# Optimization experiments

Hardware: AMD Instinct MI355X
Metric: run time of the kernel (lower is better)

## Reference

```python
import jax, jax.numpy as jnp
import numpy as np

B, T, E, A = 4, 4096, 256, 64

def setup_inputs() -> dict:
    key = jax.random.key(0)
    ks = jax.random.split(key, 7)
    s = 1.0 / np.sqrt(E)
    return {
        "embedded": jax.random.normal(ks[0], (B, T, E), dtype=jnp.float32),
        "Wk": jax.random.normal(ks[1], (E, A), dtype=jnp.float32) * s,
        "bk": jax.random.normal(ks[2], (A,), dtype=jnp.float32) * s,
        "Wq": jax.random.normal(ks[3], (E, A), dtype=jnp.float32) * s,
        "bq": jax.random.normal(ks[4], (A,), dtype=jnp.float32) * s,
        "Wv": jax.random.normal(ks[5], (E, A), dtype=jnp.float32) * s,
        "bv": jax.random.normal(ks[6], (A,), dtype=jnp.float32) * s,
    }

def reference(embedded, Wk, bk, Wq, bq, Wv, bv):
    k = embedded @ Wk + bk                      # [B,T,A]
    q = embedded @ Wq + bq
    v = embedded @ Wv + bv
    scale = 1.0 / jnp.sqrt(jnp.asarray(k.shape[-1], dtype=k.dtype))
    scores = jnp.einsum('bqa,bka->bqk', q, k) * scale   # [B,T,T]
    Tn = scores.shape[-1]
    causal = jnp.tril(jnp.ones((Tn, Tn), dtype=bool))
    scores = jnp.where(causal, scores, -jnp.inf)
    sm = jax.nn.softmax(scores, axis=-1)
    return jnp.einsum('bqk,bka->bqa', sm, v)            # [B,T,A]
```

## Files before the change

kernel.cpp:

```cpp
#include <hip/hip_runtime.h>
#include <math.h>

#define Bn 4
#define Tn 4096
#define En 256
#define An 64
#define PLS 72
#define WLS 264

typedef __attribute__((ext_vector_type(8))) short short8;
typedef __attribute__((ext_vector_type(8))) __bf16 bf16x8;
typedef __attribute__((ext_vector_type(4))) float f32x4;
typedef __attribute__((ext_vector_type(4))) short short4v;
typedef __attribute__((ext_vector_type(2))) unsigned int uint2v;

__device__ __forceinline__ f32x4 mfma16(short8 a, short8 b, f32x4 c) {
    return __builtin_amdgcn_mfma_f32_16x16x32_bf16(
        __builtin_bit_cast(bf16x8, a), __builtin_bit_cast(bf16x8, b), c, 0, 0, 0);
}
__device__ __forceinline__ unsigned short f2bf(float x) {
    unsigned int u = __builtin_bit_cast(unsigned int, x);
    u += 0x7fffu + ((u >> 16) & 1u);
    return (unsigned short)(u >> 16);
}
__device__ __forceinline__ float bf2f(unsigned short h) {
    return __builtin_bit_cast(float, (unsigned int)h << 16);
}
__device__ __forceinline__ unsigned int packbf2(float lo, float hi) {
    return (unsigned int)f2bf(lo) | ((unsigned int)f2bf(hi) << 16);
}

__global__ __launch_bounds__(256, 2) void proj_kernel(
    const float* __restrict__ emb,
    const float* __restrict__ Wq, const float* __restrict__ Wk, const float* __restrict__ Wv,
    const float* __restrict__ bq, const float* __restrict__ bk, const float* __restrict__ bv,
    unsigned short* __restrict__ qg, unsigned short* __restrict__ kg,
    unsigned short* __restrict__ v_t)
{
    const int bid  = blockIdx.x;
    const int tid  = threadIdx.x;
    const int wave = tid >> 6, lane = tid & 63, quad = lane >> 4, l15 = lane & 15;
    const int jh   = bid & 1;
    const int rb   = bid >> 1;
    const int row0  = rb * 64;
    const int b     = row0 >> 12;
    const int trow0 = row0 & 4095;

    __shared__ unsigned short Wl[96 * WLS];
    __shared__ unsigned short vtr[64 * PLS];

    {
        const float* __restrict__ srcA = jh ? Wv : Wq;
        const int lrbA = jh ? 32 : 0;
#pragma unroll
        for (int it = 0; it < 16; it++) {
            const int idx = it * 256 + tid;
            const int e   = idx >> 4;
            const int c4  = (idx & 15) * 4;
            float4 w = *(const float4*)&srcA[(size_t)e * An + c4];
            Wl[(lrbA + c4 + 0) * WLS + e] = f2bf(w.x);
            Wl[(lrbA + c4 + 1) * WLS + e] = f2bf(w.y);
            Wl[(lrbA + c4 + 2) * WLS + e] = f2bf(w.z);
            Wl[(lrbA + c4 + 3) * WLS + e] = f2bf(w.w);
        }
        const int coloff = jh ? 32 : 0;
        const int lrbB   = jh ? 0 : 64;
#pragma unroll
        for (int it = 0; it < 8; it++) {
            const int idx = it * 256 + tid;
            const int e   = idx >> 3;
            const int c4  = (idx & 7) * 4;
            float4 w = *(const float4*)&Wk[(size_t)e * An + coloff + c4];
            Wl[(lrbB + c4 + 0) * WLS + e] = f2bf(w.x);
            Wl[(lrbB + c4 + 1) * WLS + e] = f2bf(w.y);
            Wl[(lrbB + c4 + 2) * WLS + e] = f2bf(w.z);
            Wl[(lrbB + c4 + 3) * WLS + e] = f2bf(w.w);
        }
    }

    short8 A[8];
    {
        const float* erow = emb + (size_t)(row0 + wave * 16 + l15) * En;
#pragma unroll
        for (int c = 0; c < 8; c++) {
            const float* pp = erow + c * 32 + quad * 8;
            float4 f0 = *(const float4*)pp;
            float4 f1 = *(const float4*)(pp + 4);
            A[c] = (short8){(short)f2bf(f0.x), (short)f2bf(f0.y), (short)f2bf(f0.z), (short)f2bf(f0.w),
                            (short)f2bf(f1.x), (short)f2bf(f1.y), (short)f2bf(f1.z), (short)f2bf(f1.w)};
        }
    }
    __syncthreads();

    f32x4 acc[6];
#pragma unroll
    for (int x = 0; x < 6; x++) acc[x] = (f32x4){0.f, 0.f, 0.f, 0.f};

#pragma unroll
    for (int x = 0; x < 6; x++) {
        const unsigned short* wrow = &Wl[(x * 16 + l15) * WLS];
#pragma unroll
        for (int c = 0; c < 8; c++)
            acc[x] = mfma16(A[c], *(const short8*)(wrow + c * 32 + quad * 8), acc[x]);
    }

    const float QS = 0.125f * 1.4426950408889634f;
    const int row_l = wave * 16 + quad * 4;

    if (jh == 0) {
        __syncthreads();
#pragma unroll
        for (int x = 0; x < 4; x++) {
            const int al = x * 16 + l15;
            const float bsv = bq[al];
#pragma unroll
            for (int rg = 0; rg < 4; rg++)
                vtr[(row_l + rg) * PLS + al] = f2bf((acc[x][rg] + bsv) * QS);
        }
        __syncthreads();
        if (tid < 128) {
            const int row = tid >> 1, cg = (tid & 1) * 32;
            unsigned short* dst = qg + (size_t)(row0 + row) * An + cg;
            *(short8*)dst       = *(const short8*)&vtr[row * PLS + cg];
            *(short8*)(dst + 8) = *(const short8*)&vtr[row * PLS + cg + 8];
            *(short8*)(dst + 16) = *(const short8*)&vtr[row * PLS + cg + 16];
            *(short8*)(dst + 24) = *(const short8*)&vtr[row * PLS + cg + 24];
        }
        __syncthreads();
#pragma unroll
        for (int x = 4; x < 6; x++) {
            const int al = (x - 4) * 16 + l15;
            const float bsv = bk[al];
#pragma unroll
            for (int rg = 0; rg < 4; rg++)
                vtr[(row_l + rg) * PLS + al] = f2bf(acc[x][rg] + bsv);
        }
        __syncthreads();
        if (tid < 64) {
            const int row = tid;
            unsigned short* dst = kg + (size_t)(row0 + row) * An;
            *(short8*)dst       = *(const short8*)&vtr[row * PLS];
            *(short8*)(dst + 8) = *(const short8*)&vtr[row * PLS + 8];
            *(short8*)(dst + 16) = *(const short8*)&vtr[row * PLS + 16];
            *(short8*)(dst + 24) = *(const short8*)&vtr[row * PLS + 24];
        }
    } else {
        __syncthreads();
#pragma unroll
        for (int x = 0; x < 2; x++) {
            const int al = (2 + x) * 16 + l15;
            const float bsv = bk[al];
#pragma unroll
            for (int rg = 0; rg < 4; rg++)
                vtr[(row_l + rg) * PLS + al] = f2bf(acc[x][rg] + bsv);
        }
        __syncthreads();
        if (tid < 64) {
            const int row = tid;
            unsigned short* dst = kg + (size_t)(row0 + row) * An + 32;
            *(short8*)dst       = *(const short8*)&vtr[row * PLS + 32];
            *(short8*)(dst + 8) = *(const short8*)&vtr[row * PLS + 40];
            *(short8*)(dst + 16) = *(const short8*)&vtr[row * PLS + 48];
            *(short8*)(dst + 24) = *(const short8*)&vtr[row * PLS + 56];
        }
        __syncthreads();
#pragma unroll
        for (int x = 2; x < 6; x++) {
            const int al = (x - 2) * 16 + l15;
            const float bsv = bv[al];
#pragma unroll
            for (int rg = 0; rg < 4; rg++)
                vtr[al * PLS + row_l + rg] = f2bf(acc[x][rg] + bsv);
        }
        __syncthreads();
        {
            const int a  = tid >> 2;
            const int tg = (tid & 3) * 16;
            unsigned short* dst = v_t + (size_t)(b * 64 + a) * Tn + trow0 + tg;
            *(short8*)dst       = *(const short8*)&vtr[a * PLS + tg];
            *(short8*)(dst + 8) = *(const short8*)&vtr[a * PLS + tg + 8];
        }
    }
}

__global__ __launch_bounds__(256, 2) void flash_kernel(
    const unsigned short* __restrict__ qg, const unsigned short* __restrict__ kg,
    const unsigned short* __restrict__ v_t,
    unsigned short* __restrict__ Opart, float* __restrict__ ml,
    int S, int lgS)
{
    const int b    = blockIdx.y;
    const int tid  = threadIdx.x;
    const int wave = tid >> 6, lane = tid & 63, quad = lane >> 4, l15 = lane & 15;
    const int u    = blockIdx.x * 4 + wave;
    const int p    = u >> lgS;
    const int s    = u & (S - 1);

    __shared__ unsigned short lds[4 * 64 * PLS];
    unsigned short* tw = lds + wave * (64 * PLS);

    const unsigned short* kb0 = kg  + ((size_t)b << 12) * An;
    const unsigned short* vb0 = v_t + (size_t)b * An * Tn;

#pragma unroll 1
    for (int tile = 0; tile < 2; tile++) {
        const int qt    = tile ? (63 - p) : p;
        const int qrow0 = qt * 64;
        const int tmax  = qt;

        short8 qB[4][2];
        {
            const unsigned short* qb = qg + (((size_t)b << 12) + qrow0) * An;
#pragma unroll
            for (int g = 0; g < 4; g++)
#pragma unroll
                for (int c = 0; c < 2; c++)
                    qB[g][c] = *(const short8*)(qb + (size_t)(16 * g + l15) * An + c * 32 + quad * 8);
        }

        float l_lane[4] = {0.f, 0.f, 0.f, 0.f};
        f32x4 O[4][4];
#pragma unroll
        for (int nt = 0; nt < 4; nt++)
#pragma unroll
            for (int g = 0; g < 4; g++) O[nt][g] = (f32x4){0.f, 0.f, 0.f, 0.f};

        int t = s;
        if (t <= tmax) {
            short8 KA[4][2];
            {
                const unsigned short* kb = kb0 + (size_t)t * (64 * An);
#pragma unroll
                for (int nt = 0; nt < 4; nt++)
#pragma unroll
                    for (int c = 0; c < 2; c++)
                        KA[nt][c] = *(const short8*)(kb + (nt * 16 + l15) * An + c * 32 + quad * 8);
            }
            for (;;) {
                short8 VA[4][2];
                {
                    const unsigned short* vb = vb0 + (size_t)t * 64;
#pragma unroll
                    for (int nt = 0; nt < 4; nt++)
#pragma unroll
                        for (int c = 0; c < 2; c++)
                            VA[nt][c] = *(const short8*)(vb + (size_t)(nt * 16 + l15) * Tn + c * 32 + quad * 8);
                }

                const int tn = t + S;
                const bool more = (tn <= tmax);
                short8 KN[4][2];
                if (more) {
                    const unsigned short* kb = kb0 + (size_t)tn * (64 * An);
#pragma unroll
                    for (int nt = 0; nt < 4; nt++)
#pragma unroll
                        for (int c = 0; c < 2; c++)
                            KN[nt][c] = *(const short8*)(kb + (nt * 16 + l15) * An + c * 32 + quad * 8);
                }

                const bool diag = (t == tmax);

#pragma unroll
                for (int g = 0; g < 4; g++) {
                    f32x4 St[4];
#pragma unroll
                    for (int nt = 0; nt < 4; nt++) {
                        f32x4 a0 = (f32x4){0.f, 0.f, 0.f, 0.f};
                        a0 = mfma16(KA[nt][0], qB[g][0], a0);
                        a0 = mfma16(KA[nt][1], qB[g][1], a0);
                        St[nt] = a0;
                    }
                    if (diag) {
                        const int qr = 16 * g + l15;
                        const int kvb = quad * 4;
#pragma unroll
                        for (int nt = 0; nt < 4; nt++)
#pragma unroll
                            for (int rg = 0; rg < 4; rg++)
                                if (nt * 16 + kvb + rg > qr) St[nt][rg] = -__builtin_inff();
                    }
                    float rs = l_lane[g];
#pragma unroll
                    for (int nt = 0; nt < 4; nt++) {
#pragma unroll
                        for (int rg = 0; rg < 4; rg++) {
                            const float pv = exp2f(St[nt][rg]);
                            St[nt][rg] = pv;
                            rs += pv;
                        }
                        const unsigned int d0 = packbf2(St[nt][0], St[nt][1]);
                        const unsigned int d1 = packbf2(St[nt][2], St[nt][3]);
                        *(short4v*)&tw[(16 * g + l15) * PLS + 16 * nt + quad * 4] =
                            __builtin_bit_cast(short4v, (uint2v){d0, d1});
                    }
                    l_lane[g] = rs;
#pragma unroll
                    for (int c = 0; c < 2; c++) {
                        const short8 pb = *(const short8*)&tw[(16 * g + l15) * PLS + c * 32 + quad * 8];
#pragma unroll
                        for (int nt = 0; nt < 4; nt++)
                            O[nt][g] = mfma16(VA[nt][c], pb, O[nt][g]);
                    }
                }

                if (!more) break;
                t = tn;
#pragma unroll
                for (int nt = 0; nt < 4; nt++)
#pragma unroll
                    for (int c = 0; c < 2; c++) KA[nt][c] = KN[nt][c];
            }
        }

        float l_red[4];
#pragma unroll
        for (int g = 0; g < 4; g++) {
            float rs = l_lane[g];
            rs += __shfl_xor(rs, 16);
            rs += __shfl_xor(rs, 32);
            l_red[g] = rs;
        }
#pragma unroll
        for (int nt = 0; nt < 4; nt++)
#pragma unroll
            for (int g = 0; g < 4; g++) {
                const unsigned int d0 = packbf2(O[nt][g][0], O[nt][g][1]);
                const unsigned int d1 = packbf2(O[nt][g][2], O[nt][g][3]);
                *(short4v*)&tw[(16 * g + l15) * PLS + 16 * nt + quad * 4] =
                    __builtin_bit_cast(short4v, (uint2v){d0, d1});
            }
        {
            const size_t unit = (size_t)(b * 64 + qt) * (size_t)S + s;
            unsigned short* ob = Opart + unit * 4096;
#pragma unroll
            for (int rr = 0; rr < 2; rr++) {
                const int row = rr * 32 + (lane >> 1);
#pragma unroll
                for (int pp = 0; pp < 4; pp++) {
                    const int colh = (lane & 1) * 8 + pp * 16;
                    *(short8*)(ob + row * 64 + colh) = *(const short8*)&tw[row * PLS + colh];
                }
            }
            if (quad == 0) {
                float* mlb = ml + unit * 64;
#pragma unroll
                for (int g = 0; g < 4; g++)
                    mlb[16 * g + l15] = l_red[g];
            }
        }
    }
}

__global__ __launch_bounds__(256) void merge_kernel(
    const unsigned short* __restrict__ Opart, const float* __restrict__ ml,
    float* __restrict__ out, int S)
{
    const int qt = blockIdx.x, b = blockIdx.y;
    const int tid = threadIdx.x;
    const int qr  = tid >> 2;
    const int a16 = (tid & 3) * 16;
    const size_t ub = (size_t)(b * 64 + qt) * (size_t)S;

    float acc[16];
#pragma unroll
    for (int x = 0; x < 16; x++) acc[x] = 0.f;
    float lsum = 0.f;

#pragma unroll 1
    for (int s = 0; s < S; s++) {
        lsum += ml[(ub + s) * 64 + qr];
        const unsigned short* op = &Opart[(ub + s) * 4096 + qr * 64 + a16];
        const short8 o0 = *(const short8*)op;
        const short8 o1 = *(const short8*)(op + 8);
#pragma unroll
        for (int x = 0; x < 8; x++) {
            acc[x]     += bf2f((unsigned short)o0[x]);
            acc[8 + x] += bf2f((unsigned short)o1[x]);
        }
    }
    const float inv = 1.f / lsum;
    float* o = out + (((size_t)b << 12) + qt * 64 + qr) * An + a16;
#pragma unroll
    for (int h = 0; h < 4; h++) {
        float4 r = {acc[h * 4] * inv, acc[h * 4 + 1] * inv,
                    acc[h * 4 + 2] * inv, acc[h * 4 + 3] * inv};
        *(float4*)(o + h * 4) = r;
    }
}

extern "C" void kernel_launch(void* const* d_in, const int* in_sizes, int n_in,
                              void* d_out, int out_size, void* d_ws, size_t ws_size,
                              hipStream_t stream) {
    const float* emb = (const float*)d_in[0];
    const float* Wk  = (const float*)d_in[1];
    const float* bk  = (const float*)d_in[2];
    const float* Wq  = (const float*)d_in[3];
    const float* bq  = (const float*)d_in[4];
    const float* Wv  = (const float*)d_in[5];
    const float* bv  = (const float*)d_in[6];
    float* out = (float*)d_out;

    char* ws = (char*)d_ws;
    const size_t MB = 1024 * 1024;

    int S = 8, lgS = 3;
    {
        const size_t need16 = 6 * MB + 64 * 1024
                            + (size_t)16 * 64 * 1024
                            + (size_t)16 * 2 * MB;
        if (need16 <= ws_size) { S = 16; lgS = 4; }
    }

    unsigned short* q     = (unsigned short*)(ws);
    unsigned short* k     = (unsigned short*)(ws + 2 * MB);
    unsigned short* v_t   = (unsigned short*)(ws + 4 * MB);
    float*          ml    = (float*)(ws + 6 * MB + 64 * 1024);
    unsigned short* Opart = (unsigned short*)(ws + 6 * MB + 64 * 1024 + (size_t)S * 64 * 1024);

    proj_kernel<<<512, 256, 0, stream>>>(emb, Wq, Wk, Wv, bq, bk, bv, q, k, v_t);
    flash_kernel<<<dim3(8 * S, 4), 256, 0, stream>>>(q, k, v_t, Opart, ml, S, lgS);
    merge_kernel<<<dim3(64, 4), 256, 0, stream>>>(Opart, ml, out, S);
}
```

Before: 144.6 us.

## Shrink flash query tiles to 32 rows, keep P in registers with fp16 PV MFMA

The flash kernel now works on 32-row query tiles instead of 64, which doubles the number of work units and raises occupancy to 4 blocks per SM via launch bounds. V is stored as fp16 so the PV product can use the 16x16x16 f16 MFMA with P taken straight from the score accumulator registers, removing the LDS round-trip used to transpose P. Block indices are remapped to interleave batches, and the explicit K prefetch of the next tile is dropped. The merge kernel and workspace sizing are adapted to the 32-row partials. Risks include fp16 range for V and P, the loss of K prefetch overlap, and the lower-throughput K=16 MFMA.

```diff
diff --git a/kernel.cpp b/kernel.cpp
--- a/kernel.cpp
+++ b/kernel.cpp
@@ -12,11 +12,15 @@
 typedef __attribute__((ext_vector_type(8))) __bf16 bf16x8;
 typedef __attribute__((ext_vector_type(4))) float f32x4;
 typedef __attribute__((ext_vector_type(4))) short short4v;
+typedef __attribute__((ext_vector_type(4))) _Float16 f16x4;
 typedef __attribute__((ext_vector_type(2))) unsigned int uint2v;
 
 __device__ __forceinline__ f32x4 mfma16(short8 a, short8 b, f32x4 c) {
     return __builtin_amdgcn_mfma_f32_16x16x32_bf16(
         __builtin_bit_cast(bf16x8, a), __builtin_bit_cast(bf16x8, b), c, 0, 0, 0);
+}
+__device__ __forceinline__ f32x4 mfma16h(f16x4 a, f16x4 b, f32x4 c) {
+    return __builtin_amdgcn_mfma_f32_16x16x16f16(a, b, c, 0, 0, 0);
 }
 __device__ __forceinline__ unsigned short f2bf(float x) {
     unsigned int u = __builtin_bit_cast(unsigned int, x);
@@ -28,6 +32,10 @@
 }
 __device__ __forceinline__ unsigned int packbf2(float lo, float hi) {
     return (unsigned int)f2bf(lo) | ((unsigned int)f2bf(hi) << 16);
+}
+__device__ __forceinline__ unsigned short f2h(float x) {
+    _Float16 h = (_Float16)x;
+    return __builtin_bit_cast(unsigned short, h);
 }
 
 __global__ __launch_bounds__(256, 2) void proj_kernel(
@@ -121,8 +129,8 @@
         if (tid < 128) {
             const int row = tid >> 1, cg = (tid & 1) * 32;
             unsigned short* dst = qg + (size_t)(row0 + row) * An + cg;
-            *(short8*)dst       = *(const short8*)&vtr[row * PLS + cg];
-            *(short8*)(dst + 8) = *(const short8*)&vtr[row * PLS + cg + 8];
+            *(short8*)dst        = *(const short8*)&vtr[row * PLS + cg];
+            *(short8*)(dst + 8)  = *(const short8*)&vtr[row * PLS + cg + 8];
             *(short8*)(dst + 16) = *(const short8*)&vtr[row * PLS + cg + 16];
             *(short8*)(dst + 24) = *(const short8*)&vtr[row * PLS + cg + 24];
         }
@@ -139,8 +147,8 @@
         if (tid < 64) {
             const int row = tid;
             unsigned short* dst = kg + (size_t)(row0 + row) * An;
-            *(short8*)dst       = *(const short8*)&vtr[row * PLS];
-            *(short8*)(dst + 8) = *(const short8*)&vtr[row * PLS + 8];
+            *(short8*)dst        = *(const short8*)&vtr[row * PLS];
+            *(short8*)(dst + 8)  = *(const short8*)&vtr[row * PLS + 8];
             *(short8*)(dst + 16) = *(const short8*)&vtr[row * PLS + 16];
             *(short8*)(dst + 24) = *(const short8*)&vtr[row * PLS + 24];
         }
@@ -158,8 +166,8 @@
         if (tid < 64) {
             const int row = tid;
             unsigned short* dst = kg + (size_t)(row0 + row) * An + 32;
-            *(short8*)dst       = *(const short8*)&vtr[row * PLS + 32];
-            *(short8*)(dst + 8) = *(const short8*)&vtr[row * PLS + 40];
+            *(short8*)dst        = *(const short8*)&vtr[row * PLS + 32];
+            *(short8*)(dst + 8)  = *(const short8*)&vtr[row * PLS + 40];
             *(short8*)(dst + 16) = *(const short8*)&vtr[row * PLS + 48];
             *(short8*)(dst + 24) = *(const short8*)&vtr[row * PLS + 56];
         }
@@ -170,7 +178,7 @@
             const float bsv = bv[al];
 #pragma unroll
             for (int rg = 0; rg < 4; rg++)
-                vtr[al * PLS + row_l + rg] = f2bf(acc[x][rg] + bsv);
+                vtr[al * PLS + row_l + rg] = f2h(acc[x][rg] + bsv);
         }
         __syncthreads();
         {
@@ -183,50 +191,52 @@
     }
 }
 
-__global__ __launch_bounds__(256, 2) void flash_kernel(
+__global__ __launch_bounds__(256, 4) void flash_kernel(
     const unsigned short* __restrict__ qg, const unsigned short* __restrict__ kg,
     const unsigned short* __restrict__ v_t,
     unsigned short* __restrict__ Opart, float* __restrict__ ml,
     int S, int lgS)
 {
-    const int b    = blockIdx.y;
+    const int bid  = blockIdx.x;
     const int tid  = threadIdx.x;
     const int wave = tid >> 6, lane = tid & 63, quad = lane >> 4, l15 = lane & 15;
-    const int u    = blockIdx.x * 4 + wave;
+    const int b    = (bid & 7) >> 1;
+    const int idx  = (bid >> 3) * 2 + (bid & 1);
+    const int u    = idx * 4 + wave;
     const int p    = u >> lgS;
     const int s    = u & (S - 1);
 
-    __shared__ unsigned short lds[4 * 64 * PLS];
-    unsigned short* tw = lds + wave * (64 * PLS);
+    __shared__ unsigned short lds[4 * 32 * PLS];
+    unsigned short* tw = lds + wave * (32 * PLS);
 
     const unsigned short* kb0 = kg  + ((size_t)b << 12) * An;
     const unsigned short* vb0 = v_t + (size_t)b * An * Tn;
 
 #pragma unroll 1
     for (int tile = 0; tile < 2; tile++) {
-        const int qt    = tile ? (63 - p) : p;
-        const int qrow0 = qt * 64;
-        const int tmax  = qt;
-
-        short8 qB[4][2];
+        const int qt32  = tile ? (127 - p) : p;
+        const int qrow0 = qt32 * 32;
+        const int tmax  = qt32 >> 1;
+
+        short8 qB[2][2];
         {
             const unsigned short* qb = qg + (((size_t)b << 12) + qrow0) * An;
 #pragma unroll
-            for (int g = 0; g < 4; g++)
+            for (int g = 0; g < 2; g++)
 #pragma unroll
                 for (int c = 0; c < 2; c++)
                     qB[g][c] = *(const short8*)(qb + (size_t)(16 * g + l15) * An + c * 32 + quad * 8);
         }
 
-        float l_lane[4] = {0.f, 0.f, 0.f, 0.f};
-        f32x4 O[4][4];
+        float l_lane[2] = {0.f, 0.f};
+        f32x4 O[4][2];
 #pragma unroll
         for (int nt = 0; nt < 4; nt++)
 #pragma unroll
-            for (int g = 0; g < 4; g++) O[nt][g] = (f32x4){0.f, 0.f, 0.f, 0.f};
-
-        int t = s;
-        if (t <= tmax) {
+            for (int g = 0; g < 2; g++) O[nt][g] = (f32x4){0.f, 0.f, 0.f, 0.f};
+
+#pragma unroll 1
+        for (int t = s; t <= tmax; t += S) {
             short8 KA[4][2];
             {
                 const unsigned short* kb = kb0 + (size_t)t * (64 * An);
@@ -236,86 +246,70 @@
                     for (int c = 0; c < 2; c++)
                         KA[nt][c] = *(const short8*)(kb + (nt * 16 + l15) * An + c * 32 + quad * 8);
             }
-            for (;;) {
-                short8 VA[4][2];
-                {
-                    const unsigned short* vb = vb0 + (size_t)t * 64;
+
+            f32x4 St[4][2];
+#pragma unroll
+            for (int nt = 0; nt < 4; nt++)
+#pragma unroll
+                for (int g = 0; g < 2; g++) {
+                    f32x4 a0 = (f32x4){0.f, 0.f, 0.f, 0.f};
+                    a0 = mfma16(KA[nt][0], qB[g][0], a0);
+                    a0 = mfma16(KA[nt][1], qB[g][1], a0);
+                    St[nt][g] = a0;
+                }
+
+            f16x4 VA[4][4];
+            {
+                const unsigned short* vb = vb0 + (size_t)t * 64 + quad * 4;
+#pragma unroll
+                for (int nt = 0; nt < 4; nt++)
+#pragma unroll
+                    for (int kc = 0; kc < 4; kc++)
+                        VA[nt][kc] = *(const f16x4*)(vb + (size_t)(nt * 16 + l15) * Tn + kc * 16);
+            }
+
+            if (t == tmax) {
+                const int kvb = t * 64 + quad * 4;
+#pragma unroll
+                for (int nt = 0; nt < 4; nt++)
+#pragma unroll
+                    for (int g = 0; g < 2; g++) {
+                        const int qr = qrow0 + 16 * g + l15;
+#pragma unroll
+                        for (int rg = 0; rg < 4; rg++)
+                            if (kvb + nt * 16 + rg > qr) St[nt][g][rg] = -__builtin_inff();
+                    }
+            }
+
+#pragma unroll
+            for (int g = 0; g < 2; g++) {
+                float rs = l_lane[g];
+#pragma unroll
+                for (int nt = 0; nt < 4; nt++)
+#pragma unroll
+                    for (int rg = 0; rg < 4; rg++) {
+                        const float pv = exp2f(St[nt][g][rg]);
+                        St[nt][g][rg] = pv;
+                        rs += pv;
+                    }
+                l_lane[g] = rs;
+            }
+
+#pragma unroll
+            for (int kc = 0; kc < 4; kc++)
+#pragma unroll
+                for (int g = 0; g < 2; g++) {
+                    const f16x4 pb = { (_Float16)St[kc][g][0], (_Float16)St[kc][g][1],
+                                       (_Float16)St[kc][g][2], (_Float16)St[kc][g][3] };
 #pragma unroll
                     for (int nt = 0; nt < 4; nt++)
-#pragma unroll
-                        for (int c = 0; c < 2; c++)
-                            VA[nt][c] = *(const short8*)(vb + (size_t)(nt * 16 + l15) * Tn + c * 32 + quad * 8);
+                        O[nt][g] = mfma16h(VA[nt][kc], pb, O[nt][g]);
                 }
-
-                const int tn = t + S;
-                const bool more = (tn <= tmax);
-                short8 KN[4][2];
-                if (more) {
-                    const unsigned short* kb = kb0 + (size_t)tn * (64 * An);
-#pragma unroll
-                    for (int nt = 0; nt < 4; nt++)
-#pragma unroll
-                        for (int c = 0; c < 2; c++)
-                            KN[nt][c] = *(const short8*)(kb + (nt * 16 + l15) * An + c * 32 + quad * 8);
-                }
-
-                const bool diag = (t == tmax);
-
-#pragma unroll
-                for (int g = 0; g < 4; g++) {
-                    f32x4 St[4];
-#pragma unroll
-                    for (int nt = 0; nt < 4; nt++) {
-                        f32x4 a0 = (f32x4){0.f, 0.f, 0.f, 0.f};
-                        a0 = mfma16(KA[nt][0], qB[g][0], a0);
-                        a0 = mfma16(KA[nt][1], qB[g][1], a0);
-                        St[nt] = a0;
-                    }
-                    if (diag) {
-                        const int qr = 16 * g + l15;
-                        const int kvb = quad * 4;
-#pragma unroll
-                        for (int nt = 0; nt < 4; nt++)
-#pragma unroll
-                            for (int rg = 0; rg < 4; rg++)
-                                if (nt * 16 + kvb + rg > qr) St[nt][rg] = -__builtin_inff();
-                    }
-                    float rs = l_lane[g];
-#pragma unroll
-                    for (int nt = 0; nt < 4; nt++) {
-#pragma unroll
-                        for (int rg = 0; rg < 4; rg++) {
-                            const float pv = exp2f(St[nt][rg]);
-                            St[nt][rg] = pv;
-                            rs += pv;
-                        }
-                        const unsigned int d0 = packbf2(St[nt][0], St[nt][1]);
-                        const unsigned int d1 = packbf2(St[nt][2], St[nt][3]);
-                        *(short4v*)&tw[(16 * g + l15) * PLS + 16 * nt + quad * 4] =
-                            __builtin_bit_cast(short4v, (uint2v){d0, d1});
-                    }
-                    l_lane[g] = rs;
-#pragma unroll
-                    for (int c = 0; c < 2; c++) {
-                        const short8 pb = *(const short8*)&tw[(16 * g + l15) * PLS + c * 32 + quad * 8];
-#pragma unroll
-                        for (int nt = 0; nt < 4; nt++)
-                            O[nt][g] = mfma16(VA[nt][c], pb, O[nt][g]);
-                    }
-                }
-
-                if (!more) break;
-                t = tn;
-#pragma unroll
-                for (int nt = 0; nt < 4; nt++)
-#pragma unroll
-                    for (int c = 0; c < 2; c++) KA[nt][c] = KN[nt][c];
-            }
-        }
-
-        float l_red[4];
-#pragma unroll
-        for (int g = 0; g < 4; g++) {
+        }
+
+        float l_red[2];
+#pragma unroll
+        for (int g = 0; g < 2; g++) {
             float rs = l_lane[g];
             rs += __shfl_xor(rs, 16);
             rs += __shfl_xor(rs, 32);
@@ -324,28 +318,25 @@
 #pragma unroll
         for (int nt = 0; nt < 4; nt++)
 #pragma unroll
-            for (int g = 0; g < 4; g++) {
+            for (int g = 0; g < 2; g++) {
                 const unsigned int d0 = packbf2(O[nt][g][0], O[nt][g][1]);
                 const unsigned int d1 = packbf2(O[nt][g][2], O[nt][g][3]);
                 *(short4v*)&tw[(16 * g + l15) * PLS + 16 * nt + quad * 4] =
                     __builtin_bit_cast(short4v, (uint2v){d0, d1});
             }
         {
-            const size_t unit = (size_t)(b * 64 + qt) * (size_t)S + s;
-            unsigned short* ob = Opart + unit * 4096;
-#pragma unroll
-            for (int rr = 0; rr < 2; rr++) {
-                const int row = rr * 32 + (lane >> 1);
-#pragma unroll
-                for (int pp = 0; pp < 4; pp++) {
-                    const int colh = (lane & 1) * 8 + pp * 16;
-                    *(short8*)(ob + row * 64 + colh) = *(const short8*)&tw[row * PLS + colh];
-                }
+            const size_t unit = (size_t)(b * 128 + qt32) * (size_t)S + s;
+            unsigned short* ob = Opart + unit * 2048;
+            const int row = lane >> 1;
+#pragma unroll
+            for (int pp = 0; pp < 4; pp++) {
+                const int colh = (lane & 1) * 8 + pp * 16;
+                *(short8*)(ob + row * 64 + colh) = *(const short8*)&tw[row * PLS + colh];
             }
             if (quad == 0) {
-                float* mlb = ml + unit * 64;
-#pragma unroll
-                for (int g = 0; g < 4; g++)
+                float* mlb = ml + unit * 32;
+#pragma unroll
+                for (int g = 0; g < 2; g++)
                     mlb[16 * g + l15] = l_red[g];
             }
         }
@@ -356,37 +347,30 @@
     const unsigned short* __restrict__ Opart, const float* __restrict__ ml,
     float* __restrict__ out, int S)
 {
-    const int qt = blockIdx.x, b = blockIdx.y;
+    const int qt32 = blockIdx.x, b = blockIdx.y;
     const int tid = threadIdx.x;
-    const int qr  = tid >> 2;
-    const int a16 = (tid & 3) * 16;
-    const size_t ub = (size_t)(b * 64 + qt) * (size_t)S;
-
-    float acc[16];
-#pragma unroll
-    for (int x = 0; x < 16; x++) acc[x] = 0.f;
+    const int qr  = tid >> 3;
+    const int a8  = (tid & 7) * 8;
+    const size_t ub = (size_t)(b * 128 + qt32) * (size_t)S;
+
+    float acc[8];
+#pragma unroll
+    for (int x = 0; x < 8; x++) acc[x] = 0.f;
     float lsum = 0.f;
 
 #pragma unroll 1
     for (int s = 0; s < S; s++) {
-        lsum += ml[(ub + s) * 64 + qr];
-        const unsigned short* op = &Opart[(ub + s) * 4096 + qr * 64 + a16];
-        const short8 o0 = *(const short8*)op;
-        const short8 o1 = *(const short8*)(op + 8);
-#pragma unroll
-        for (int x = 0; x < 8; x++) {
-            acc[x]     += bf2f((unsigned short)o0[x]);
-            acc[8 + x] += bf2f((unsigned short)o1[x]);
-        }
+        lsum += ml[(ub + s) * 32 + qr];
+        const short8 ov = *(const short8*)&Opart[(ub + s) * 2048 + qr * 64 + a8];
+#pragma unroll
+        for (int x = 0; x < 8; x++) acc[x] += bf2f((unsigned short)ov[x]);
     }
     const float inv = 1.f / lsum;
-    float* o = out + (((size_t)b << 12) + qt * 64 + qr) * An + a16;
-#pragma unroll
-    for (int h = 0; h < 4; h++) {
-        float4 r = {acc[h * 4] * inv, acc[h * 4 + 1] * inv,
-                    acc[h * 4 + 2] * inv, acc[h * 4 + 3] * inv};
-        *(float4*)(o + h * 4) = r;
-    }
+    float* o = out + (((size_t)b << 12) + qt32 * 32 + qr) * An + a8;
+    float4 r0 = {acc[0] * inv, acc[1] * inv, acc[2] * inv, acc[3] * inv};
+    float4 r1 = {acc[4] * inv, acc[5] * inv, acc[6] * inv, acc[7] * inv};
+    *(float4*)o       = r0;
+    *(float4*)(o + 4) = r1;
 }
 
 extern "C" void kernel_launch(void* const* d_in, const int* in_sizes, int n_in,
@@ -407,8 +391,8 @@
     int S = 8, lgS = 3;
     {
         const size_t need16 = 6 * MB + 64 * 1024
-                            + (size_t)16 * 64 * 1024
-                            + (size_t)16 * 2 * MB;
+                            + (size_t)512 * 16 * 128
+                            + (size_t)512 * 16 * 4096;
         if (need16 <= ws_size) { S = 16; lgS = 4; }
     }
 
@@ -416,9 +400,9 @@
     unsigned short* k     = (unsigned short*)(ws + 2 * MB);
     unsigned short* v_t   = (unsigned short*)(ws + 4 * MB);
     float*          ml    = (float*)(ws + 6 * MB + 64 * 1024);
-    unsigned short* Opart = (unsigned short*)(ws + 6 * MB + 64 * 1024 + (size_t)S * 64 * 1024);
+    unsigned short* Opart = (unsigned short*)(ws + 6 * MB + 64 * 1024 + (size_t)512 * S * 128);
 
     proj_kernel<<<512, 256, 0, stream>>>(emb, Wq, Wk, Wv, bq, bk, bv, q, k, v_t);
-    flash_kernel<<<dim3(8 * S, 4), 256, 0, stream>>>(q, k, v_t, Opart, ml, S, lgS);
-    merge_kernel<<<dim3(64, 4), 256, 0, stream>>>(Opart, ml, out, S);
-}
+    flash_kernel<<<64 * S, 256, 0, stream>>>(q, k, v_t, Opart, ml, S, lgS);
+    merge_kernel<<<dim3(128, 4), 256, 0, stream>>>(Opart, ml, out, S);
+}
```

Measured after the change: 171.0 us. 18.3% more time.

## Split KV into 32 chunks with online softmax and in-block partial merge

Applied to the files above, without the earlier changes.

Each flash block now handles one q-tile pair with 32 KV splits: its four waves each take a different split, and their partial results are merged in LDS with running-max rescaling before one partial per block goes to global memory. The kernel switches from a max-free exp to an online softmax with per-row max tracking, and the global merge kernel reads 8 partials instead of up to 16. The aim is more parallelism per q-tile and less partial-output traffic. The cost is extra shuffles, rescaling work and two block-level barriers.

```diff
diff --git a/kernel.cpp b/kernel.cpp
--- a/kernel.cpp
+++ b/kernel.cpp
@@ -5,6 +5,7 @@
 #define Tn 4096
 #define En 256
 #define An 64
+#define SS 32
 #define PLS 72
 #define WLS 264
 
@@ -121,8 +122,8 @@
         if (tid < 128) {
             const int row = tid >> 1, cg = (tid & 1) * 32;
             unsigned short* dst = qg + (size_t)(row0 + row) * An + cg;
-            *(short8*)dst       = *(const short8*)&vtr[row * PLS + cg];
-            *(short8*)(dst + 8) = *(const short8*)&vtr[row * PLS + cg + 8];
+            *(short8*)dst        = *(const short8*)&vtr[row * PLS + cg];
+            *(short8*)(dst + 8)  = *(const short8*)&vtr[row * PLS + cg + 8];
             *(short8*)(dst + 16) = *(const short8*)&vtr[row * PLS + cg + 16];
             *(short8*)(dst + 24) = *(const short8*)&vtr[row * PLS + cg + 24];
         }
@@ -139,8 +140,8 @@
         if (tid < 64) {
             const int row = tid;
             unsigned short* dst = kg + (size_t)(row0 + row) * An;
-            *(short8*)dst       = *(const short8*)&vtr[row * PLS];
-            *(short8*)(dst + 8) = *(const short8*)&vtr[row * PLS + 8];
+            *(short8*)dst        = *(const short8*)&vtr[row * PLS];
+            *(short8*)(dst + 8)  = *(const short8*)&vtr[row * PLS + 8];
             *(short8*)(dst + 16) = *(const short8*)&vtr[row * PLS + 16];
             *(short8*)(dst + 24) = *(const short8*)&vtr[row * PLS + 24];
         }
@@ -158,8 +159,8 @@
         if (tid < 64) {
             const int row = tid;
             unsigned short* dst = kg + (size_t)(row0 + row) * An + 32;
-            *(short8*)dst       = *(const short8*)&vtr[row * PLS + 32];
-            *(short8*)(dst + 8) = *(const short8*)&vtr[row * PLS + 40];
+            *(short8*)dst        = *(const short8*)&vtr[row * PLS + 32];
+            *(short8*)(dst + 8)  = *(const short8*)&vtr[row * PLS + 40];
             *(short8*)(dst + 16) = *(const short8*)&vtr[row * PLS + 48];
             *(short8*)(dst + 24) = *(const short8*)&vtr[row * PLS + 56];
         }
@@ -186,17 +187,18 @@
 __global__ __launch_bounds__(256, 2) void flash_kernel(
     const unsigned short* __restrict__ qg, const unsigned short* __restrict__ kg,
     const unsigned short* __restrict__ v_t,
-    unsigned short* __restrict__ Opart, float* __restrict__ ml,
-    int S, int lgS)
+    unsigned short* __restrict__ Opart, float* __restrict__ ml)
 {
     const int b    = blockIdx.y;
     const int tid  = threadIdx.x;
     const int wave = tid >> 6, lane = tid & 63, quad = lane >> 4, l15 = lane & 15;
-    const int u    = blockIdx.x * 4 + wave;
-    const int p    = u >> lgS;
-    const int s    = u & (S - 1);
+    const int bx   = blockIdx.x;
+    const int p    = bx >> 3;
+    const int jj   = bx & 7;
+    const int sid  = jj * 4 + wave;
 
     __shared__ unsigned short lds[4 * 64 * PLS];
+    __shared__ float mlds[4][2][64];
     unsigned short* tw = lds + wave * (64 * PLS);
 
     const unsigned short* kb0 = kg  + ((size_t)b << 12) * An;
@@ -218,14 +220,15 @@
                     qB[g][c] = *(const short8*)(qb + (size_t)(16 * g + l15) * An + c * 32 + quad * 8);
         }
 
-        float l_lane[4] = {0.f, 0.f, 0.f, 0.f};
+        float m_s[4] = {-__builtin_inff(), -__builtin_inff(), -__builtin_inff(), -__builtin_inff()};
+        float l_s[4] = {0.f, 0.f, 0.f, 0.f};
         f32x4 O[4][4];
 #pragma unroll
         for (int nt = 0; nt < 4; nt++)
 #pragma unroll
             for (int g = 0; g < 4; g++) O[nt][g] = (f32x4){0.f, 0.f, 0.f, 0.f};
 
-        int t = s;
+        int t = sid;
         if (t <= tmax) {
             short8 KA[4][2];
             {
@@ -247,7 +250,7 @@
                             VA[nt][c] = *(const short8*)(vb + (size_t)(nt * 16 + l15) * Tn + c * 32 + quad * 8);
                 }
 
-                const int tn = t + S;
+                const int tn = t + SS;
                 const bool more = (tn <= tmax);
                 short8 KN[4][2];
                 if (more) {
@@ -280,12 +283,22 @@
                             for (int rg = 0; rg < 4; rg++)
                                 if (nt * 16 + kvb + rg > qr) St[nt][rg] = -__builtin_inff();
                     }
-                    float rs = l_lane[g];
+                    float mt = -__builtin_inff();
+#pragma unroll
+                    for (int nt = 0; nt < 4; nt++)
+                        mt = fmaxf(mt, fmaxf(fmaxf(St[nt][0], St[nt][1]),
+                                             fmaxf(St[nt][2], St[nt][3])));
+                    mt = fmaxf(mt, __shfl_xor(mt, 16));
+                    mt = fmaxf(mt, __shfl_xor(mt, 32));
+                    const float mn = fmaxf(m_s[g], mt);
+                    const float alpha = exp2f(m_s[g] - mn);
+                    m_s[g] = mn;
+                    float rs = 0.f;
 #pragma unroll
                     for (int nt = 0; nt < 4; nt++) {
 #pragma unroll
                         for (int rg = 0; rg < 4; rg++) {
-                            const float pv = exp2f(St[nt][rg]);
+                            const float pv = exp2f(St[nt][rg] - mn);
                             St[nt][rg] = pv;
                             rs += pv;
                         }
@@ -294,7 +307,15 @@
                         *(short4v*)&tw[(16 * g + l15) * PLS + 16 * nt + quad * 4] =
                             __builtin_bit_cast(short4v, (uint2v){d0, d1});
                     }
-                    l_lane[g] = rs;
+                    rs += __shfl_xor(rs, 16);
+                    rs += __shfl_xor(rs, 32);
+                    l_s[g] = l_s[g] * alpha + rs;
+                    if (!__all(alpha == 1.f)) {
+#pragma unroll
+                        for (int nt = 0; nt < 4; nt++)
+#pragma unroll
+                            for (int rg = 0; rg < 4; rg++) O[nt][g][rg] *= alpha;
+                    }
 #pragma unroll
                     for (int c = 0; c < 2; c++) {
                         const short8 pb = *(const short8*)&tw[(16 * g + l15) * PLS + c * 32 + quad * 8];
@@ -313,14 +334,6 @@
             }
         }
 
-        float l_red[4];
-#pragma unroll
-        for (int g = 0; g < 4; g++) {
-            float rs = l_lane[g];
-            rs += __shfl_xor(rs, 16);
-            rs += __shfl_xor(rs, 32);
-            l_red[g] = rs;
-        }
 #pragma unroll
         for (int nt = 0; nt < 4; nt++)
 #pragma unroll
@@ -330,37 +343,83 @@
                 *(short4v*)&tw[(16 * g + l15) * PLS + 16 * nt + quad * 4] =
                     __builtin_bit_cast(short4v, (uint2v){d0, d1});
             }
+        if (quad == 0) {
+#pragma unroll
+            for (int g = 0; g < 4; g++) {
+                mlds[wave][0][16 * g + l15] = m_s[g];
+                mlds[wave][1][16 * g + l15] = l_s[g];
+            }
+        }
+        __syncthreads();
+
         {
-            const size_t unit = (size_t)(b * 64 + qt) * (size_t)S + s;
-            unsigned short* ob = Opart + unit * 4096;
-#pragma unroll
-            for (int rr = 0; rr < 2; rr++) {
-                const int row = rr * 32 + (lane >> 1);
-#pragma unroll
-                for (int pp = 0; pp < 4; pp++) {
-                    const int colh = (lane & 1) * 8 + pp * 16;
-                    *(short8*)(ob + row * 64 + colh) = *(const short8*)&tw[row * PLS + colh];
+            const int r   = tid >> 2;
+            const int c16 = (tid & 3) * 16;
+            float mw[4], lw[4];
+#pragma unroll
+            for (int w = 0; w < 4; w++) { mw[w] = mlds[w][0][r]; lw[w] = mlds[w][1][r]; }
+            const float mstar = fmaxf(fmaxf(mw[0], mw[1]), fmaxf(mw[2], mw[3]));
+            float acc[16];
+#pragma unroll
+            for (int x = 0; x < 16; x++) acc[x] = 0.f;
+            float lsum = 0.f;
+#pragma unroll
+            for (int w = 0; w < 4; w++) {
+                const float wsf = (mw[w] == -__builtin_inff()) ? 0.f : exp2f(mw[w] - mstar);
+                lsum += lw[w] * wsf;
+                if (wsf != 0.f) {
+                    const unsigned short* tp = &lds[w * 64 * PLS + r * PLS + c16];
+                    const short8 o0 = *(const short8*)tp;
+                    const short8 o1 = *(const short8*)(tp + 8);
+#pragma unroll
+                    for (int x = 0; x < 8; x++) {
+                        acc[x]     += wsf * bf2f((unsigned short)o0[x]);
+                        acc[8 + x] += wsf * bf2f((unsigned short)o1[x]);
+                    }
                 }
             }
-            if (quad == 0) {
-                float* mlb = ml + unit * 64;
-#pragma unroll
-                for (int g = 0; g < 4; g++)
-                    mlb[16 * g + l15] = l_red[g];
-            }
-        }
+            const size_t unit = (size_t)(b * 64 + qt) * 8 + jj;
+            unsigned short* ob = Opart + unit * 4096 + r * 64 + c16;
+            short4v s0 = __builtin_bit_cast(short4v,
+                (uint2v){packbf2(acc[0], acc[1]), packbf2(acc[2], acc[3])});
+            short4v s1 = __builtin_bit_cast(short4v,
+                (uint2v){packbf2(acc[4], acc[5]), packbf2(acc[6], acc[7])});
+            short4v s2 = __builtin_bit_cast(short4v,
+                (uint2v){packbf2(acc[8], acc[9]), packbf2(acc[10], acc[11])});
+            short4v s3 = __builtin_bit_cast(short4v,
+                (uint2v){packbf2(acc[12], acc[13]), packbf2(acc[14], acc[15])});
+            *(short4v*)ob       = s0;
+            *(short4v*)(ob + 4) = s1;
+            *(short4v*)(ob + 8) = s2;
+            *(short4v*)(ob + 12) = s3;
+            if ((tid & 3) == 0) {
+                ml[unit * 128 + r]      = mstar;
+                ml[unit * 128 + 64 + r] = lsum;
+            }
+        }
+        __syncthreads();
     }
 }
 
 __global__ __launch_bounds__(256) void merge_kernel(
     const unsigned short* __restrict__ Opart, const float* __restrict__ ml,
-    float* __restrict__ out, int S)
+    float* __restrict__ out)
 {
     const int qt = blockIdx.x, b = blockIdx.y;
     const int tid = threadIdx.x;
-    const int qr  = tid >> 2;
-    const int a16 = (tid & 3) * 16;
-    const size_t ub = (size_t)(b * 64 + qt) * (size_t)S;
+    const int r   = tid >> 2;
+    const int c16 = (tid & 3) * 16;
+    const size_t ub = (size_t)(b * 64 + qt) * 8;
+
+    float mw[8], lw[8];
+#pragma unroll
+    for (int j = 0; j < 8; j++) {
+        mw[j] = ml[(ub + j) * 128 + r];
+        lw[j] = ml[(ub + j) * 128 + 64 + r];
+    }
+    float mstar = -__builtin_inff();
+#pragma unroll
+    for (int j = 0; j < 8; j++) mstar = fmaxf(mstar, mw[j]);
 
     float acc[16];
 #pragma unroll
@@ -368,24 +427,27 @@
     float lsum = 0.f;
 
 #pragma unroll 1
-    for (int s = 0; s < S; s++) {
-        lsum += ml[(ub + s) * 64 + qr];
-        const unsigned short* op = &Opart[(ub + s) * 4096 + qr * 64 + a16];
-        const short8 o0 = *(const short8*)op;
-        const short8 o1 = *(const short8*)(op + 8);
-#pragma unroll
-        for (int x = 0; x < 8; x++) {
-            acc[x]     += bf2f((unsigned short)o0[x]);
-            acc[8 + x] += bf2f((unsigned short)o1[x]);
+    for (int j = 0; j < 8; j++) {
+        const float wsf = (mw[j] == -__builtin_inff()) ? 0.f : exp2f(mw[j] - mstar);
+        lsum += lw[j] * wsf;
+        if (wsf != 0.f) {
+            const unsigned short* op = &Opart[(ub + j) * 4096 + r * 64 + c16];
+            const short8 o0 = *(const short8*)op;
+            const short8 o1 = *(const short8*)(op + 8);
+#pragma unroll
+            for (int x = 0; x < 8; x++) {
+                acc[x]     += wsf * bf2f((unsigned short)o0[x]);
+                acc[8 + x] += wsf * bf2f((unsigned short)o1[x]);
+            }
         }
     }
     const float inv = 1.f / lsum;
-    float* o = out + (((size_t)b << 12) + qt * 64 + qr) * An + a16;
+    float* o = out + (((size_t)b << 12) + qt * 64 + r) * An + c16;
 #pragma unroll
     for (int h = 0; h < 4; h++) {
-        float4 r = {acc[h * 4] * inv, acc[h * 4 + 1] * inv,
-                    acc[h * 4 + 2] * inv, acc[h * 4 + 3] * inv};
-        *(float4*)(o + h * 4) = r;
+        float4 rr = {acc[h * 4] * inv, acc[h * 4 + 1] * inv,
+                     acc[h * 4 + 2] * inv, acc[h * 4 + 3] * inv};
+        *(float4*)(o + h * 4) = rr;
     }
 }
 
@@ -403,22 +465,13 @@
 
     char* ws = (char*)d_ws;
     const size_t MB = 1024 * 1024;
-
-    int S = 8, lgS = 3;
-    {
-        const size_t need16 = 6 * MB + 64 * 1024
-                            + (size_t)16 * 64 * 1024
-                            + (size_t)16 * 2 * MB;
-        if (need16 <= ws_size) { S = 16; lgS = 4; }
-    }
-
     unsigned short* q     = (unsigned short*)(ws);
     unsigned short* k     = (unsigned short*)(ws + 2 * MB);
     unsigned short* v_t   = (unsigned short*)(ws + 4 * MB);
-    float*          ml    = (float*)(ws + 6 * MB + 64 * 1024);
-    unsigned short* Opart = (unsigned short*)(ws + 6 * MB + 64 * 1024 + (size_t)S * 64 * 1024);
+    float*          ml    = (float*)(ws + 6 * MB);
+    unsigned short* Opart = (unsigned short*)(ws + 7 * MB);
 
     proj_kernel<<<512, 256, 0, stream>>>(emb, Wq, Wk, Wv, bq, bk, bv, q, k, v_t);
-    flash_kernel<<<dim3(8 * S, 4), 256, 0, stream>>>(q, k, v_t, Opart, ml, S, lgS);
-    merge_kernel<<<dim3(64, 4), 256, 0, stream>>>(Opart, ml, out, S);
-}
+    flash_kernel<<<dim3(256, 4), 256, 0, stream>>>(q, k, v_t, Opart, ml);
+    merge_kernel<<<dim3(64, 4), 256, 0, stream>>>(Opart, ml, out);
+}
```

After: 144.5 us. About the same (-0.1%).
